# Kernel optimization log

Measured on AMD Instinct MI355X. Metric: run time of the kernel, lower is better.

## Reference

```python
import jax, jax.numpy as jnp
import numpy as np

B, CIN, L = 16, 256, 2048
HID, G, M = 512, 2, 512
LP = L // 2  # pooled length == hidden_length of patterns
BETA = 1.0


def setup_inputs() -> dict:
    key = jax.random.key(0)
    k = jax.random.split(key, 6)
    x = jax.random.normal(k[0], (B, CIN, L), dtype=jnp.float32)
    # ChannelPool: Conv1d(256 -> 512, kernel=1, groups=2): weight [512, 128, 1]
    w1 = jax.random.normal(k[1], (HID, CIN // G, 1), dtype=jnp.float32) * 0.05
    b1 = jax.random.normal(k[2], (HID,), dtype=jnp.float32) * 0.01
    # StatePattern memory bank: [num_memories, hidden_length]
    patterns = jax.random.normal(k[3], (M, LP), dtype=jnp.float32) * 0.02
    # Unpool: ConvTranspose1d(512 -> 256, kernel=2, stride=2, groups=2):
    # torch weight layout [in_channels, out_channels//groups, kernel] = [512, 128, 2]
    wT = jax.random.normal(k[4], (HID, CIN // G, 2), dtype=jnp.float32) * 0.05
    bT = jax.random.normal(k[5], (CIN,), dtype=jnp.float32) * 0.01
    RZ = jnp.array(0.1, dtype=jnp.float32)
    return {"x": x, "w1": w1, "b1": b1, "patterns": patterns, "wT": wT, "bT": bT, "RZ": RZ}


def reference(x, w1, b1, patterns, wT, bT, RZ):
    identity = x
    # --- grouped 1x1 conv (ChannelPool) ---
    # split channels into G groups: x [B,G,CIN/G,L], w [G,HID/G,CIN/G]
    xg = x.reshape(B, G, CIN // G, L)
    wg = w1[:, :, 0].reshape(G, HID // G, CIN // G)
    h = jnp.einsum('bgil,goi->bgol', xg, wg).reshape(B, HID, L) + b1[None, :, None]
    h = jax.nn.relu(h)  # act; norm1/dropout are identity (norm=False, eval)
    # --- MaxPool1d(kernel=2, stride=2) ---
    h = h.reshape(B, HID, LP, 2).max(axis=-1)  # [B, HID, LP]
    # --- Hopfield retrieval: softmax(beta * x @ P^T) @ P ---
    scores = jnp.einsum('bcl,ml->bcm', BETA * h, patterns)  # [B, HID, M]
    attn = jax.nn.softmax(scores, axis=-1)
    h = jnp.einsum('bcm,ml->bcl', attn, patterns)  # [B, HID, LP]
    # --- grouped ConvTranspose1d(k=2, s=2) ---
    hg = h.reshape(B, G, HID // G, LP)
    wtg = wT.reshape(G, HID // G, CIN // G, 2)
    y = jnp.einsum('bgil,giok->bgolk', hg, wtg)  # [B,G,CIN/G,LP,2]
    y = y.reshape(B, CIN, L) + bT[None, :, None]
    y = jax.nn.relu(y)  # act; norm2/dropout identity
    return identity + RZ * y
```

## Files before the change

kernel.cpp:

```cpp
#include <hip/hip_runtime.h>

#define NB 16
#define NCIN 256
#define NL 2048
#define NHID 512
#define NM 512
#define NLP 1024
#define BK 64

typedef short bf16x8 __attribute__((ext_vector_type(8)));
typedef unsigned short u16x8 __attribute__((ext_vector_type(8)));
typedef float f32x4 __attribute__((ext_vector_type(4)));
typedef __attribute__((address_space(1))) const unsigned int gas_u32;
typedef __attribute__((address_space(3))) unsigned int las_u32;

__device__ __forceinline__ unsigned short f2bf(float f) {
    unsigned int u = __builtin_bit_cast(unsigned int, f);
    return (unsigned short)((u + 0x7FFFu + ((u >> 16) & 1u)) >> 16);
}

__global__ __launch_bounds__(256) void k_prep(
    const float* __restrict__ P, unsigned short* __restrict__ Pb,
    unsigned short* __restrict__ Ptb)
{
    __shared__ unsigned short tbuf[64][65];
    const int mt = blockIdx.x >> 4;
    const int lt = blockIdx.x & 15;
    for (int i = threadIdx.x; i < 4096; i += 256) {
        const int r = i >> 6, c = i & 63;
        const unsigned short b = f2bf(P[(size_t)(mt * 64 + r) * 1024 + lt * 64 + c]);
        Pb[(size_t)(mt * 64 + r) * 1024 + lt * 64 + c] = b;
        tbuf[c][r] = b;
    }
    __syncthreads();
    for (int i = threadIdx.x; i < 4096; i += 256) {
        const int r = i >> 6, c = i & 63;
        Ptb[(size_t)(lt * 64 + r) * 512 + mt * 64 + c] = tbuf[r][c];
    }
}

__global__ __launch_bounds__(256) void k_prep2(
    const float* __restrict__ w1, const float* __restrict__ wT,
    unsigned short* __restrict__ w1b, unsigned short* __restrict__ wTt)
{
    const int t = blockIdx.x * 256 + threadIdx.x;
    if (t < 65536) w1b[t] = f2bf(w1[t]);
    if (t < 131072) {
        const int g = t >> 16, ok = (t >> 8) & 255, i = t & 255;
        wTt[t] = f2bf(wT[((size_t)(g * 256 + i)) * 256 + ok]);
    }
}

__global__ __launch_bounds__(256) void k0_xT(
    const float* __restrict__ x, unsigned short* __restrict__ xT)
{
    const int ct = blockIdx.x & 3;
    const int lt = (blockIdx.x >> 2) & 31;
    const int b  = blockIdx.x >> 7;
    __shared__ float tile[64 * 68];
    const int t = threadIdx.x;
    #pragma unroll
    for (int it = 0; it < 4; ++it) {
        const int idx = t + it * 256;
        const int ch = idx >> 4, f4 = idx & 15;
        const float4 v = *(const float4*)(x + ((size_t)(b * 256 + ct * 64 + ch)) * 2048 + lt * 64 + f4 * 4);
        *(float4*)(tile + ch * 68 + f4 * 4) = v;
    }
    __syncthreads();
    const int l = t >> 2, cq = t & 3;
    u16x8 o0, o1;
    #pragma unroll
    for (int k = 0; k < 8; ++k) o0[k] = f2bf(tile[(cq * 16 + k) * 68 + l]);
    #pragma unroll
    for (int k = 0; k < 8; ++k) o1[k] = f2bf(tile[(cq * 16 + 8 + k) * 68 + l]);
    unsigned short* dst = xT + ((size_t)(b * 2048 + lt * 64 + l)) * 256 + ct * 64 + cq * 16;
    *(u16x8*)dst = o0;
    *(u16x8*)(dst + 8) = o1;
}

__global__ __launch_bounds__(256) void k1_gemm(
    const unsigned short* __restrict__ xT, const unsigned short* __restrict__ w1b,
    const float* __restrict__ b1, unsigned short* __restrict__ h)
{
    const int nt = blockIdx.x & 1;
    const int g  = (blockIdx.x >> 1) & 1;
    const int rt = blockIdx.x >> 2;
    const int r0 = rt * 128;
    const int b  = r0 >> 11, l0 = r0 & 2047;
    const int c0 = g * 256 + nt * 128;

    __shared__ unsigned short Asl[128 * BK];
    __shared__ unsigned short Bsl[128 * BK];
    __shared__ unsigned short epi[128 * 72];

    const int t = threadIdx.x;
    const int lane = t & 63;
    const int wave = t >> 6;
    const int wm = wave & 1, wn = wave >> 1;
    const int q = lane >> 4, lm = lane & 15;

    f32x4 acc[4][4];
    #pragma unroll
    for (int i = 0; i < 4; ++i)
        #pragma unroll
        for (int j = 0; j < 4; ++j)
            #pragma unroll
            for (int r = 0; r < 4; ++r) acc[i][j][r] = 0.f;

    for (int k0 = 0; k0 < 128; k0 += BK) {
        #pragma unroll
        for (int rd = 0; rd < 4; ++rd) {
            const int e = rd * 2048 + t * 8;
            const int row = e >> 6, col = e & 63;
            const unsigned short* ga = xT + (size_t)(r0 + row) * 256 + g * 128 + k0 + col;
            __builtin_amdgcn_global_load_lds((gas_u32*)ga, (las_u32*)(Asl + e), 16, 0, 0);
            const unsigned short* gb = w1b + (size_t)(c0 + row) * 128 + k0 + col;
            __builtin_amdgcn_global_load_lds((gas_u32*)gb, (las_u32*)(Bsl + e), 16, 0, 0);
        }
        __syncthreads();
        #pragma unroll
        for (int kk = 0; kk < 2; ++kk) {
            bf16x8 af[4], bf[4];
            #pragma unroll
            for (int i = 0; i < 4; ++i)
                af[i] = *(const bf16x8*)(Asl + (wm * 64 + i * 16 + lm) * BK + kk * 32 + q * 8);
            #pragma unroll
            for (int j = 0; j < 4; ++j)
                bf[j] = *(const bf16x8*)(Bsl + (wn * 64 + j * 16 + lm) * BK + kk * 32 + q * 8);
            #pragma unroll
            for (int i = 0; i < 4; ++i)
                #pragma unroll
                for (int j = 0; j < 4; ++j)
                    acc[i][j] = __builtin_amdgcn_mfma_f32_16x16x32_bf16(af[i], bf[j], acc[i][j], 0, 0, 0);
        }
        __syncthreads();
    }

    #pragma unroll
    for (int j = 0; j < 4; ++j) {
        const int c_blk = wn * 64 + j * 16 + lm;
        const float bias = b1[c0 + c_blk];
        #pragma unroll
        for (int i = 0; i < 4; ++i) {
            const float p0 = fmaxf(fmaxf(acc[i][j][0], acc[i][j][1]) + bias, 0.f);
            const float p1 = fmaxf(fmaxf(acc[i][j][2], acc[i][j][3]) + bias, 0.f);
            const int lp_blk = wm * 32 + i * 8 + q * 2;
            ushort2 u; u.x = f2bf(p0); u.y = f2bf(p1);
            *(ushort2*)(epi + c_blk * 72 + lp_blk) = u;
        }
    }
    __syncthreads();
    const int c_blk = t >> 1, half = t & 1;
    unsigned short* dst = h + ((size_t)(b * 512 + c0 + c_blk)) * 1024 + (l0 >> 1) + half * 32;
    #pragma unroll
    for (int u = 0; u < 4; ++u)
        *(u16x8*)(dst + u * 8) = *(const u16x8*)(epi + c_blk * 72 + half * 32 + u * 8);
}

__global__ __launch_bounds__(256) void gemm_bt(
    const unsigned short* __restrict__ A, const unsigned short* __restrict__ B,
    float* __restrict__ C, int M, int N, int K, int ntiles)
{
    const int nt = blockIdx.x % ntiles;
    const int rt = blockIdx.x / ntiles;
    const int r0 = rt * 128, n0 = nt * 128;

    __shared__ unsigned short Asl[128 * BK];
    __shared__ unsigned short Bsl[128 * BK];

    const int t = threadIdx.x;
    const int lane = t & 63;
    const int wave = t >> 6;
    const int wm = wave & 1, wn = wave >> 1;
    const int q = lane >> 4, lm = lane & 15;

    f32x4 acc[4][4];
    #pragma unroll
    for (int i = 0; i < 4; ++i)
        #pragma unroll
        for (int j = 0; j < 4; ++j)
            #pragma unroll
            for (int r = 0; r < 4; ++r) acc[i][j][r] = 0.f;

    for (int k0 = 0; k0 < K; k0 += BK) {
        #pragma unroll
        for (int rd = 0; rd < 4; ++rd) {
            const int e = rd * 2048 + t * 8;
            const int row = e >> 6, col = e & 63;
            const unsigned short* ga = A + (size_t)(r0 + row) * K + k0 + col;
            __builtin_amdgcn_global_load_lds((gas_u32*)ga, (las_u32*)(Asl + e), 16, 0, 0);
            const unsigned short* gb = B + (size_t)(n0 + row) * K + k0 + col;
            __builtin_amdgcn_global_load_lds((gas_u32*)gb, (las_u32*)(Bsl + e), 16, 0, 0);
        }
        __syncthreads();
        #pragma unroll
        for (int kk = 0; kk < 2; ++kk) {
            bf16x8 af[4], bf[4];
            #pragma unroll
            for (int i = 0; i < 4; ++i)
                af[i] = *(const bf16x8*)(Asl + (wm * 64 + i * 16 + lm) * BK + kk * 32 + q * 8);
            #pragma unroll
            for (int j = 0; j < 4; ++j)
                bf[j] = *(const bf16x8*)(Bsl + (wn * 64 + j * 16 + lm) * BK + kk * 32 + q * 8);
            #pragma unroll
            for (int i = 0; i < 4; ++i)
                #pragma unroll
                for (int j = 0; j < 4; ++j)
                    acc[i][j] = __builtin_amdgcn_mfma_f32_16x16x32_bf16(af[i], bf[j], acc[i][j], 0, 0, 0);
        }
        __syncthreads();
    }

    #pragma unroll
    for (int i = 0; i < 4; ++i)
        #pragma unroll
        for (int j = 0; j < 4; ++j)
            #pragma unroll
            for (int r = 0; r < 4; ++r)
                C[(size_t)(r0 + wm * 64 + i * 16 + q * 4 + r) * N + n0 + wn * 64 + j * 16 + lm] = acc[i][j][r];
}

__global__ __launch_bounds__(256) void k_softmax(
    const float* __restrict__ S, unsigned short* __restrict__ Ab)
{
    const int row = blockIdx.x * 4 + (threadIdx.x >> 6);
    const int lane = threadIdx.x & 63;
    const float* p = S + (size_t)row * 512;
    unsigned short* po = Ab + (size_t)row * 512;

    float v[8];
    #pragma unroll
    for (int j = 0; j < 8; ++j) v[j] = p[lane + 64 * j];

    float mx = v[0];
    #pragma unroll
    for (int j = 1; j < 8; ++j) mx = fmaxf(mx, v[j]);
    for (int off = 32; off > 0; off >>= 1) mx = fmaxf(mx, __shfl_xor(mx, off));

    float sum = 0.f;
    #pragma unroll
    for (int j = 0; j < 8; ++j) { v[j] = __expf(v[j] - mx); sum += v[j]; }
    for (int off = 32; off > 0; off >>= 1) sum += __shfl_xor(sum, off);

    const float inv = 1.f / sum;
    #pragma unroll
    for (int j = 0; j < 8; ++j) po[lane + 64 * j] = f2bf(v[j] * inv);
}

__global__ __launch_bounds__(256) void gemm_retr(
    const unsigned short* __restrict__ Ptb, const unsigned short* __restrict__ Ab,
    unsigned short* __restrict__ h2T)
{
    const int tl = blockIdx.x & 31;
    const int b  = blockIdx.x >> 5;
    const int nt = tl & 3;
    const int rt = tl >> 2;
    const int r0 = rt * 128, n0 = nt * 128;

    __shared__ unsigned short Asl[128 * BK];
    __shared__ unsigned short Bsl[128 * BK];

    const int t = threadIdx.x;
    const int lane = t & 63;
    const int wave = t >> 6;
    const int wm = wave & 1, wn = wave >> 1;
    const int q = lane >> 4, lm = lane & 15;

    f32x4 acc[4][4];
    #pragma unroll
    for (int i = 0; i < 4; ++i)
        #pragma unroll
        for (int j = 0; j < 4; ++j)
            #pragma unroll
            for (int r = 0; r < 4; ++r) acc[i][j][r] = 0.f;

    for (int k0 = 0; k0 < 512; k0 += BK) {
        #pragma unroll
        for (int rd = 0; rd < 4; ++rd) {
            const int e = rd * 2048 + t * 8;
            const int row = e >> 6, col = e & 63;
            const unsigned short* ga = Ptb + (size_t)(r0 + row) * 512 + k0 + col;
            __builtin_amdgcn_global_load_lds((gas_u32*)ga, (las_u32*)(Asl + e), 16, 0, 0);
            const unsigned short* gb = Ab + ((size_t)b * 512 + n0 + row) * 512 + k0 + col;
            __builtin_amdgcn_global_load_lds((gas_u32*)gb, (las_u32*)(Bsl + e), 16, 0, 0);
        }
        __syncthreads();
        #pragma unroll
        for (int kk = 0; kk < 2; ++kk) {
            bf16x8 af[4], bf[4];
            #pragma unroll
            for (int i = 0; i < 4; ++i)
                af[i] = *(const bf16x8*)(Asl + (wm * 64 + i * 16 + lm) * BK + kk * 32 + q * 8);
            #pragma unroll
            for (int j = 0; j < 4; ++j)
                bf[j] = *(const bf16x8*)(Bsl + (wn * 64 + j * 16 + lm) * BK + kk * 32 + q * 8);
            #pragma unroll
            for (int i = 0; i < 4; ++i)
                #pragma unroll
                for (int j = 0; j < 4; ++j)
                    acc[i][j] = __builtin_amdgcn_mfma_f32_16x16x32_bf16(af[i], bf[j], acc[i][j], 0, 0, 0);
        }
        __syncthreads();
    }

    #pragma unroll
    for (int i = 0; i < 4; ++i)
        #pragma unroll
        for (int j = 0; j < 4; ++j)
            #pragma unroll
            for (int r = 0; r < 4; ++r)
                h2T[((size_t)b * 1024 + r0 + wm * 64 + i * 16 + q * 4 + r) * 512
                    + n0 + wn * 64 + j * 16 + lm] = f2bf(acc[i][j][r]);
}

__global__ __launch_bounds__(256) void k4_gemm(
    const unsigned short* __restrict__ h2T, const unsigned short* __restrict__ wTt,
    const float* __restrict__ bT, const float* __restrict__ x,
    const float* __restrict__ RZ, float* __restrict__ out)
{
    const int nt = blockIdx.x & 1;
    const int g  = (blockIdx.x >> 1) & 1;
    const int rt = blockIdx.x >> 2;
    const int r0 = rt * 128;
    const int b  = r0 >> 10, lp0 = r0 & 1023;

    __shared__ __align__(16) char smem[65536];
    unsigned short* Asl = (unsigned short*)smem;
    unsigned short* Bsl = Asl + 128 * BK;
    float* epi = (float*)smem;

    const int t = threadIdx.x;
    const int lane = t & 63;
    const int wave = t >> 6;
    const int wm = wave & 1, wn = wave >> 1;
    const int q = lane >> 4, lm = lane & 15;

    f32x4 acc[4][4];
    #pragma unroll
    for (int i = 0; i < 4; ++i)
        #pragma unroll
        for (int j = 0; j < 4; ++j)
            #pragma unroll
            for (int r = 0; r < 4; ++r) acc[i][j][r] = 0.f;

    for (int k0 = 0; k0 < 256; k0 += BK) {
        #pragma unroll
        for (int rd = 0; rd < 4; ++rd) {
            const int e = rd * 2048 + t * 8;
            const int row = e >> 6, col = e & 63;
            const unsigned short* ga = h2T + (size_t)(r0 + row) * 512 + g * 256 + k0 + col;
            __builtin_amdgcn_global_load_lds((gas_u32*)ga, (las_u32*)(Asl + e), 16, 0, 0);
            const unsigned short* gb = wTt + (size_t)g * 65536 + (size_t)(nt * 128 + row) * 256 + k0 + col;
            __builtin_amdgcn_global_load_lds((gas_u32*)gb, (las_u32*)(Bsl + e), 16, 0, 0);
        }
        __syncthreads();
        #pragma unroll
        for (int kk = 0; kk < 2; ++kk) {
            bf16x8 af[4], bf[4];
            #pragma unroll
            for (int i = 0; i < 4; ++i)
                af[i] = *(const bf16x8*)(Asl + (wm * 64 + i * 16 + lm) * BK + kk * 32 + q * 8);
            #pragma unroll
            for (int j = 0; j < 4; ++j)
                bf[j] = *(const bf16x8*)(Bsl + (wn * 64 + j * 16 + lm) * BK + kk * 32 + q * 8);
            #pragma unroll
            for (int i = 0; i < 4; ++i)
                #pragma unroll
                for (int j = 0; j < 4; ++j)
                    acc[i][j] = __builtin_amdgcn_mfma_f32_16x16x32_bf16(af[i], bf[j], acc[i][j], 0, 0, 0);
        }
        __syncthreads();
    }

    #pragma unroll
    for (int j = 0; j < 4; ++j) {
        const int col_blk = wn * 64 + j * 16 + lm;
        const int o_l = col_blk >> 1, kk2 = col_blk & 1;
        #pragma unroll
        for (int i = 0; i < 4; ++i) {
            #pragma unroll
            for (int r = 0; r < 4; ++r) {
                const int row_l = wm * 64 + i * 16 + q * 4 + r;
                const int l_l = 2 * row_l + kk2;
                const int chunk = ((l_l >> 2) + o_l) & 63;
                epi[o_l * 256 + chunk * 4 + (l_l & 3)] = acc[i][j][r];
            }
        }
    }
    __syncthreads();
    const int row = t >> 2, quad = t & 3;
    const int c = g * 128 + nt * 64 + row;
    const float bias = bT[c];
    const float rz = RZ[0];
    const size_t gbase = ((size_t)(b * 256 + c)) * 2048 + 2 * lp0 + quad * 64;
    #pragma unroll
    for (int k = 0; k < 16; ++k) {
        const int chunk_phys = (quad * 16 + k + row) & 63;
        const float4 v = *(const float4*)(epi + row * 256 + chunk_phys * 4);
        const float4 xv = *(const float4*)(x + gbase + k * 4);
        float4 o;
        o.x = xv.x + rz * fmaxf(v.x + bias, 0.f);
        o.y = xv.y + rz * fmaxf(v.y + bias, 0.f);
        o.z = xv.z + rz * fmaxf(v.z + bias, 0.f);
        o.w = xv.w + rz * fmaxf(v.w + bias, 0.f);
        *(float4*)(out + gbase + k * 4) = o;
    }
}

extern "C" void kernel_launch(void* const* d_in, const int* in_sizes, int n_in,
                              void* d_out, int out_size, void* d_ws, size_t ws_size,
                              hipStream_t stream) {
    (void)in_sizes; (void)n_in; (void)out_size; (void)ws_size;
    const float* x  = (const float*)d_in[0];
    const float* w1 = (const float*)d_in[1];
    const float* b1 = (const float*)d_in[2];
    const float* P  = (const float*)d_in[3];
    const float* wT = (const float*)d_in[4];
    const float* bT = (const float*)d_in[5];
    const float* RZ = (const float*)d_in[6];
    float* out = (float*)d_out;

    char* ws = (char*)d_ws;
    unsigned short* xT  = (unsigned short*)ws;
    unsigned short* h2T = (unsigned short*)ws;
    unsigned short* hb  = (unsigned short*)(ws + (16u << 20));
    unsigned short* Ab  = (unsigned short*)(ws + (16u << 20));
    unsigned short* Pb  = (unsigned short*)(ws + (32u << 20));
    unsigned short* Ptb = (unsigned short*)(ws + (33u << 20));
    unsigned short* w1b = (unsigned short*)(ws + (34u << 20));
    unsigned short* wTt = (unsigned short*)(ws + (34u << 20) + (256u << 10));
    float* S = out;

    hipLaunchKernelGGL(k_prep,    dim3(128),  dim3(256), 0, stream, P, Pb, Ptb);
    hipLaunchKernelGGL(k_prep2,   dim3(512),  dim3(256), 0, stream, w1, wT, w1b, wTt);
    hipLaunchKernelGGL(k0_xT,     dim3(2048), dim3(256), 0, stream, x, xT);
    hipLaunchKernelGGL(k1_gemm,   dim3(1024), dim3(256), 0, stream, xT, w1b, b1, hb);
    hipLaunchKernelGGL(gemm_bt,   dim3(256),  dim3(256), 0, stream, hb, Pb, S,
                       8192, 512, 1024, 4);
    hipLaunchKernelGGL(k_softmax, dim3(2048), dim3(256), 0, stream, S, Ab);
    hipLaunchKernelGGL(gemm_retr, dim3(512),  dim3(256), 0, stream, Ptb, Ab, h2T);
    hipLaunchKernelGGL(k4_gemm,   dim3(512),  dim3(256), 0, stream, h2T, wTt, bT, x, RZ, out);
}
```

Measured before the change: 187.5 us.

## Widen score/retrieval GEMMs to 512 threads, store scores as bf16, merge prep kernels

Merges the two weight-preparation kernels into one launch. The score GEMM and the retrieval GEMM now use 512-thread blocks with 8 waves, each wave owning a 64x32 sub-tile, which halves accumulator registers per wave and raises occupancy. Scores are written as bf16 instead of fp32, halving the traffic into softmax, and softmax now does vectorized 16-byte loads and stores. Rounding scores to bf16 before softmax reduces accuracy of the attention weights.

Result: no change. 186.9 us (-0.3%).

```diff
diff --git a/kernel.cpp b/kernel.cpp
--- a/kernel.cpp
+++ b/kernel.cpp
@@ -18,36 +18,39 @@
     unsigned int u = __builtin_bit_cast(unsigned int, f);
     return (unsigned short)((u + 0x7FFFu + ((u >> 16) & 1u)) >> 16);
 }
+__device__ __forceinline__ float bf2f(unsigned short u) {
+    return __builtin_bit_cast(float, ((unsigned int)u) << 16);
+}
 
 __global__ __launch_bounds__(256) void k_prep(
-    const float* __restrict__ P, unsigned short* __restrict__ Pb,
-    unsigned short* __restrict__ Ptb)
+    const float* __restrict__ P, const float* __restrict__ w1,
+    const float* __restrict__ wT, unsigned short* __restrict__ Pb,
+    unsigned short* __restrict__ Ptb, unsigned short* __restrict__ w1b,
+    unsigned short* __restrict__ wTt)
 {
     __shared__ unsigned short tbuf[64][65];
-    const int mt = blockIdx.x >> 4;
-    const int lt = blockIdx.x & 15;
-    for (int i = threadIdx.x; i < 4096; i += 256) {
-        const int r = i >> 6, c = i & 63;
-        const unsigned short b = f2bf(P[(size_t)(mt * 64 + r) * 1024 + lt * 64 + c]);
-        Pb[(size_t)(mt * 64 + r) * 1024 + lt * 64 + c] = b;
-        tbuf[c][r] = b;
-    }
-    __syncthreads();
-    for (int i = threadIdx.x; i < 4096; i += 256) {
-        const int r = i >> 6, c = i & 63;
-        Ptb[(size_t)(lt * 64 + r) * 512 + mt * 64 + c] = tbuf[r][c];
-    }
-}
-
-__global__ __launch_bounds__(256) void k_prep2(
-    const float* __restrict__ w1, const float* __restrict__ wT,
-    unsigned short* __restrict__ w1b, unsigned short* __restrict__ wTt)
-{
-    const int t = blockIdx.x * 256 + threadIdx.x;
-    if (t < 65536) w1b[t] = f2bf(w1[t]);
-    if (t < 131072) {
-        const int g = t >> 16, ok = (t >> 8) & 255, i = t & 255;
-        wTt[t] = f2bf(wT[((size_t)(g * 256 + i)) * 256 + ok]);
+    const int bb = blockIdx.x;
+    if (bb < 128) {
+        const int mt = bb >> 4;
+        const int lt = bb & 15;
+        for (int i = threadIdx.x; i < 4096; i += 256) {
+            const int r = i >> 6, c = i & 63;
+            const unsigned short b = f2bf(P[(size_t)(mt * 64 + r) * 1024 + lt * 64 + c]);
+            Pb[(size_t)(mt * 64 + r) * 1024 + lt * 64 + c] = b;
+            tbuf[c][r] = b;
+        }
+        __syncthreads();
+        for (int i = threadIdx.x; i < 4096; i += 256) {
+            const int r = i >> 6, c = i & 63;
+            Ptb[(size_t)(lt * 64 + r) * 512 + mt * 64 + c] = tbuf[r][c];
+        }
+    } else {
+        const int t = (bb - 128) * 256 + threadIdx.x;
+        if (t < 65536) w1b[t] = f2bf(w1[t]);
+        if (t < 131072) {
+            const int g = t >> 16, ok = (t >> 8) & 255, i = t & 255;
+            wTt[t] = f2bf(wT[((size_t)(g * 256 + i)) * 256 + ok]);
+        }
     }
 }
 
@@ -157,12 +160,12 @@
         *(u16x8*)(dst + u * 8) = *(const u16x8*)(epi + c_blk * 72 + half * 32 + u * 8);
 }
 
-__global__ __launch_bounds__(256) void gemm_bt(
+__global__ __launch_bounds__(512, 2) void gemm_sc(
     const unsigned short* __restrict__ A, const unsigned short* __restrict__ B,
-    float* __restrict__ C, int M, int N, int K, int ntiles)
-{
-    const int nt = blockIdx.x % ntiles;
-    const int rt = blockIdx.x / ntiles;
+    unsigned short* __restrict__ Sb)
+{
+    const int nt = blockIdx.x & 3;
+    const int rt = blockIdx.x >> 2;
     const int r0 = rt * 128, n0 = nt * 128;
 
     __shared__ unsigned short Asl[128 * BK];
@@ -174,38 +177,38 @@
     const int wm = wave & 1, wn = wave >> 1;
     const int q = lane >> 4, lm = lane & 15;
 
-    f32x4 acc[4][4];
-    #pragma unroll
-    for (int i = 0; i < 4; ++i)
-        #pragma unroll
-        for (int j = 0; j < 4; ++j)
+    f32x4 acc[4][2];
+    #pragma unroll
+    for (int i = 0; i < 4; ++i)
+        #pragma unroll
+        for (int j = 0; j < 2; ++j)
             #pragma unroll
             for (int r = 0; r < 4; ++r) acc[i][j][r] = 0.f;
 
-    for (int k0 = 0; k0 < K; k0 += BK) {
-        #pragma unroll
-        for (int rd = 0; rd < 4; ++rd) {
-            const int e = rd * 2048 + t * 8;
+    for (int k0 = 0; k0 < 1024; k0 += BK) {
+        #pragma unroll
+        for (int rd = 0; rd < 2; ++rd) {
+            const int e = rd * 4096 + t * 8;
             const int row = e >> 6, col = e & 63;
-            const unsigned short* ga = A + (size_t)(r0 + row) * K + k0 + col;
+            const unsigned short* ga = A + (size_t)(r0 + row) * 1024 + k0 + col;
             __builtin_amdgcn_global_load_lds((gas_u32*)ga, (las_u32*)(Asl + e), 16, 0, 0);
-            const unsigned short* gb = B + (size_t)(n0 + row) * K + k0 + col;
+            const unsigned short* gb = B + (size_t)(n0 + row) * 1024 + k0 + col;
             __builtin_amdgcn_global_load_lds((gas_u32*)gb, (las_u32*)(Bsl + e), 16, 0, 0);
         }
         __syncthreads();
         #pragma unroll
         for (int kk = 0; kk < 2; ++kk) {
-            bf16x8 af[4], bf[4];
+            bf16x8 af[4], bf[2];
             #pragma unroll
             for (int i = 0; i < 4; ++i)
                 af[i] = *(const bf16x8*)(Asl + (wm * 64 + i * 16 + lm) * BK + kk * 32 + q * 8);
             #pragma unroll
-            for (int j = 0; j < 4; ++j)
-                bf[j] = *(const bf16x8*)(Bsl + (wn * 64 + j * 16 + lm) * BK + kk * 32 + q * 8);
+            for (int j = 0; j < 2; ++j)
+                bf[j] = *(const bf16x8*)(Bsl + (wn * 32 + j * 16 + lm) * BK + kk * 32 + q * 8);
             #pragma unroll
             for (int i = 0; i < 4; ++i)
                 #pragma unroll
-                for (int j = 0; j < 4; ++j)
+                for (int j = 0; j < 2; ++j)
                     acc[i][j] = __builtin_amdgcn_mfma_f32_16x16x32_bf16(af[i], bf[j], acc[i][j], 0, 0, 0);
         }
         __syncthreads();
@@ -214,23 +217,23 @@
     #pragma unroll
     for (int i = 0; i < 4; ++i)
         #pragma unroll
-        for (int j = 0; j < 4; ++j)
+        for (int j = 0; j < 2; ++j)
             #pragma unroll
             for (int r = 0; r < 4; ++r)
-                C[(size_t)(r0 + wm * 64 + i * 16 + q * 4 + r) * N + n0 + wn * 64 + j * 16 + lm] = acc[i][j][r];
+                Sb[(size_t)(r0 + wm * 64 + i * 16 + q * 4 + r) * 512
+                   + n0 + wn * 32 + j * 16 + lm] = f2bf(acc[i][j][r]);
 }
 
 __global__ __launch_bounds__(256) void k_softmax(
-    const float* __restrict__ S, unsigned short* __restrict__ Ab)
+    const unsigned short* __restrict__ Sb, unsigned short* __restrict__ Ab)
 {
     const int row = blockIdx.x * 4 + (threadIdx.x >> 6);
     const int lane = threadIdx.x & 63;
-    const float* p = S + (size_t)row * 512;
-    unsigned short* po = Ab + (size_t)row * 512;
+    const u16x8 uv = *(const u16x8*)(Sb + (size_t)row * 512 + lane * 8);
 
     float v[8];
     #pragma unroll
-    for (int j = 0; j < 8; ++j) v[j] = p[lane + 64 * j];
+    for (int j = 0; j < 8; ++j) v[j] = bf2f(uv[j]);
 
     float mx = v[0];
     #pragma unroll
@@ -243,11 +246,13 @@
     for (int off = 32; off > 0; off >>= 1) sum += __shfl_xor(sum, off);
 
     const float inv = 1.f / sum;
-    #pragma unroll
-    for (int j = 0; j < 8; ++j) po[lane + 64 * j] = f2bf(v[j] * inv);
-}
-
-__global__ __launch_bounds__(256) void gemm_retr(
+    u16x8 ov;
+    #pragma unroll
+    for (int j = 0; j < 8; ++j) ov[j] = f2bf(v[j] * inv);
+    *(u16x8*)(Ab + (size_t)row * 512 + lane * 8) = ov;
+}
+
+__global__ __launch_bounds__(512, 4) void gemm_retr(
     const unsigned short* __restrict__ Ptb, const unsigned short* __restrict__ Ab,
     unsigned short* __restrict__ h2T)
 {
@@ -266,18 +271,18 @@
     const int wm = wave & 1, wn = wave >> 1;
     const int q = lane >> 4, lm = lane & 15;
 
-    f32x4 acc[4][4];
-    #pragma unroll
-    for (int i = 0; i < 4; ++i)
-        #pragma unroll
-        for (int j = 0; j < 4; ++j)
+    f32x4 acc[4][2];
+    #pragma unroll
+    for (int i = 0; i < 4; ++i)
+        #pragma unroll
+        for (int j = 0; j < 2; ++j)
             #pragma unroll
             for (int r = 0; r < 4; ++r) acc[i][j][r] = 0.f;
 
     for (int k0 = 0; k0 < 512; k0 += BK) {
         #pragma unroll
-        for (int rd = 0; rd < 4; ++rd) {
-            const int e = rd * 2048 + t * 8;
+        for (int rd = 0; rd < 2; ++rd) {
+            const int e = rd * 4096 + t * 8;
             const int row = e >> 6, col = e & 63;
             const unsigned short* ga = Ptb + (size_t)(r0 + row) * 512 + k0 + col;
             __builtin_amdgcn_global_load_lds((gas_u32*)ga, (las_u32*)(Asl + e), 16, 0, 0);
@@ -287,17 +292,17 @@
         __syncthreads();
         #pragma unroll
         for (int kk = 0; kk < 2; ++kk) {
-            bf16x8 af[4], bf[4];
+            bf16x8 af[4], bf[2];
             #pragma unroll
             for (int i = 0; i < 4; ++i)
                 af[i] = *(const bf16x8*)(Asl + (wm * 64 + i * 16 + lm) * BK + kk * 32 + q * 8);
             #pragma unroll
-            for (int j = 0; j < 4; ++j)
-                bf[j] = *(const bf16x8*)(Bsl + (wn * 64 + j * 16 + lm) * BK + kk * 32 + q * 8);
+            for (int j = 0; j < 2; ++j)
+                bf[j] = *(const bf16x8*)(Bsl + (wn * 32 + j * 16 + lm) * BK + kk * 32 + q * 8);
             #pragma unroll
             for (int i = 0; i < 4; ++i)
                 #pragma unroll
-                for (int j = 0; j < 4; ++j)
+                for (int j = 0; j < 2; ++j)
                     acc[i][j] = __builtin_amdgcn_mfma_f32_16x16x32_bf16(af[i], bf[j], acc[i][j], 0, 0, 0);
         }
         __syncthreads();
@@ -306,11 +311,11 @@
     #pragma unroll
     for (int i = 0; i < 4; ++i)
         #pragma unroll
-        for (int j = 0; j < 4; ++j)
+        for (int j = 0; j < 2; ++j)
             #pragma unroll
             for (int r = 0; r < 4; ++r)
                 h2T[((size_t)b * 1024 + r0 + wm * 64 + i * 16 + q * 4 + r) * 512
-                    + n0 + wn * 64 + j * 16 + lm] = f2bf(acc[i][j][r]);
+                    + n0 + wn * 32 + j * 16 + lm] = f2bf(acc[i][j][r]);
 }
 
 __global__ __launch_bounds__(256) void k4_gemm(
@@ -429,15 +434,13 @@
     unsigned short* Ptb = (unsigned short*)(ws + (33u << 20));
     unsigned short* w1b = (unsigned short*)(ws + (34u << 20));
     unsigned short* wTt = (unsigned short*)(ws + (34u << 20) + (256u << 10));
-    float* S = out;
-
-    hipLaunchKernelGGL(k_prep,    dim3(128),  dim3(256), 0, stream, P, Pb, Ptb);
-    hipLaunchKernelGGL(k_prep2,   dim3(512),  dim3(256), 0, stream, w1, wT, w1b, wTt);
+    unsigned short* Sb  = (unsigned short*)out;
+
+    hipLaunchKernelGGL(k_prep,    dim3(640),  dim3(256), 0, stream, P, w1, wT, Pb, Ptb, w1b, wTt);
     hipLaunchKernelGGL(k0_xT,     dim3(2048), dim3(256), 0, stream, x, xT);
     hipLaunchKernelGGL(k1_gemm,   dim3(1024), dim3(256), 0, stream, xT, w1b, b1, hb);
-    hipLaunchKernelGGL(gemm_bt,   dim3(256),  dim3(256), 0, stream, hb, Pb, S,
-                       8192, 512, 1024, 4);
-    hipLaunchKernelGGL(k_softmax, dim3(2048), dim3(256), 0, stream, S, Ab);
-    hipLaunchKernelGGL(gemm_retr, dim3(512),  dim3(256), 0, stream, Ptb, Ab, h2T);
+    hipLaunchKernelGGL(gemm_sc,   dim3(256),  dim3(512), 0, stream, hb, Pb, Sb);
+    hipLaunchKernelGGL(k_softmax, dim3(2048), dim3(256), 0, stream, Sb, Ab);
+    hipLaunchKernelGGL(gemm_retr, dim3(512),  dim3(512), 0, stream, Ptb, Ab, h2T);
     hipLaunchKernelGGL(k4_gemm,   dim3(512),  dim3(256), 0, stream, h2T, wTt, bT, x, RZ, out);
 }
```
